# Kernel optimization log

Hardware: AMD Instinct MI355X
Metric: run time of the kernel (lower is better)

The kernel has to match this reference:

```python
import jax, jax.numpy as jnp
import numpy as np

COMMITMENT_COST = 0.25


def _l2norm(v, axis=-1, eps=1e-12):
    # matches F.normalize(p=2): v / max(||v||, eps)
    n = jnp.sqrt(jnp.sum(v * v, axis=axis, keepdims=True))
    return v / jnp.maximum(n, eps)


def setup_inputs() -> dict:
    key = jax.random.key(0)
    k1, k2 = jax.random.split(key)
    x = jax.random.normal(k1, (32768, 512), dtype=jnp.float32)
    emb_weight = jax.random.normal(k2, (8192, 512), dtype=jnp.float32)
    return {"x": x, "emb_weight": emb_weight}


def reference(x, emb_weight):
    xn = _l2norm(x)                     # [N, D]
    wn = _l2norm(emb_weight)            # [K, D]
    # squared L2 distances: ||xn||^2 + ||wn||^2 - 2 xn.wn
    dists = (jnp.sum(xn * xn, axis=-1, keepdims=True)
             + jnp.sum(wn * wn, axis=-1)
             - 2.0 * jnp.matmul(xn, wn.T))          # [N, K]
    encoding_indices = jnp.argmin(dists, axis=1)    # [N]
    quantized = _l2norm(emb_weight[encoding_indices])  # [N, D]
    q_latent_loss = jnp.mean((quantized - jax.lax.stop_gradient(xn)) ** 2)
    e_latent_loss = jnp.mean((xn - jax.lax.stop_gradient(quantized)) ** 2)
    loss = q_latent_loss + COMMITMENT_COST * e_latent_loss
    # straight-through estimator
    quantized_out = xn + jax.lax.stop_gradient(quantized - xn)
    return quantized_out, loss, encoding_indices
```

## Files before the change

kernel.cpp:

```cpp
#include <hip/hip_runtime.h>
#include <math.h>
#include <stdint.h>

#define N_Q 32768
#define K_C 8192
#define D_DIM 512
#define NSTEP 16
#define KT 64

typedef __attribute__((ext_vector_type(8))) short bf16x8;
typedef __attribute__((ext_vector_type(4))) float f32x4;
typedef unsigned long long u64;

typedef const __attribute__((address_space(1))) void gv_t;
typedef __attribute__((address_space(3))) void lv_t;

static __device__ __forceinline__ void gl16(const void* g, void* l) {
    __builtin_amdgcn_global_load_lds((gv_t*)g, (lv_t*)l, 16, 0, 0);
}

static __device__ __forceinline__ unsigned short f2bf(float f) {
    unsigned u = __float_as_uint(f);
    unsigned r = u + 0x7fffu + ((u >> 16) & 1u);
    return (unsigned short)(r >> 16);
}
static __device__ __forceinline__ float bf2f(unsigned short h) {
    return __uint_as_float(((unsigned)h) << 16);
}
static __device__ __forceinline__ unsigned fmap(float f) {
    unsigned u = __float_as_uint(f);
    return (u & 0x80000000u) ? ~u : (u | 0x80000000u);
}
static __device__ __forceinline__ float funmap(unsigned m) {
    return __uint_as_float((m & 0x80000000u) ? (m & 0x7fffffffu) : ~m);
}
static __device__ __forceinline__ u64 u64min(u64 a, u64 b) { return a < b ? a : b; }

__global__ void k_normw(const float* __restrict__ w, unsigned short* __restrict__ wh,
                        float* __restrict__ wnorm, float* __restrict__ wnorm2,
                        float* __restrict__ rho_w) {
    __shared__ float red[4];
    __shared__ float s_n;
    int k = blockIdx.x;
    int t = threadIdx.x;
    int lane = t & 63, wid = t >> 6;
    float v0 = w[(size_t)k * D_DIM + t];
    float v1 = w[(size_t)k * D_DIM + t + 256];
    float ss = fmaf(v0, v0, v1 * v1);
    for (int off = 32; off; off >>= 1) ss += __shfl_down(ss, off, 64);
    if (lane == 0) red[wid] = ss;
    __syncthreads();
    if (t == 0) s_n = fmaxf(sqrtf(red[0] + red[1] + red[2] + red[3]), 1e-12f);
    __syncthreads();
    float n = s_n;
    float a0 = v0 / n, a1 = v1 / n;
    unsigned short h0 = f2bf(a0), h1 = f2bf(a1);
    wh[(size_t)k * D_DIM + t] = h0;
    wh[(size_t)k * D_DIM + t + 256] = h1;
    float r0 = a0 - bf2f(h0), r1 = a1 - bf2f(h1);
    float s2 = fmaf(a0, a0, a1 * a1);
    float sr = fmaf(r0, r0, r1 * r1);
    for (int off = 32; off; off >>= 1) s2 += __shfl_down(s2, off, 64);
    for (int off = 32; off; off >>= 1) sr += __shfl_down(sr, off, 64);
    __syncthreads();
    if (lane == 0) red[wid] = s2;
    __syncthreads();
    float tot2 = red[0] + red[1] + red[2] + red[3];
    __syncthreads();
    if (lane == 0) red[wid] = sr;
    __syncthreads();
    if (t == 0) {
        wnorm[k] = n;
        wnorm2[k] = tot2;
        rho_w[k] = sqrtf(red[0] + red[1] + red[2] + red[3]);
    }
}

__global__ void k_wmax(const float* __restrict__ rho_w, float* __restrict__ rwmax) {
    __shared__ float red[4];
    int t = threadIdx.x, lane = t & 63, wid = t >> 6;
    float m = 0.f;
    for (int i = t; i < K_C; i += 256) m = fmaxf(m, rho_w[i]);
    for (int off = 32; off; off >>= 1) m = fmaxf(m, __shfl_down(m, off, 64));
    if (lane == 0) red[wid] = m;
    __syncthreads();
    if (t == 0) rwmax[0] = fmaxf(fmaxf(red[0], red[1]), fmaxf(red[2], red[3]));
}

__global__ void k_normx(const float* __restrict__ x, const float* __restrict__ rwmax,
                        float* __restrict__ xnorm, unsigned short* __restrict__ xh,
                        float* __restrict__ weps) {
    int wid = threadIdx.x >> 6, lane = threadIdx.x & 63;
    int n = blockIdx.x * 4 + wid;
    const float* xr = x + (size_t)n * D_DIM;
    float v[8];
    float ss = 0.f;
    #pragma unroll
    for (int i = 0; i < 8; ++i) {
        v[i] = xr[lane + i * 64];
        ss = fmaf(v[i], v[i], ss);
    }
    for (int off = 32; off; off >>= 1) ss += __shfl_down(ss, off, 64);
    ss = __shfl(ss, 0, 64);
    float nrm = fmaxf(sqrtf(ss), 1e-12f);
    float sr = 0.f;
    #pragma unroll
    for (int i = 0; i < 8; ++i) {
        float a = v[i] / nrm;
        unsigned short h = f2bf(a);
        xh[(size_t)n * D_DIM + lane + i * 64] = h;
        float r = a - bf2f(h);
        sr = fmaf(r, r, sr);
    }
    for (int off = 32; off; off >>= 1) sr += __shfl_down(sr, off, 64);
    if (lane == 0) {
        xnorm[n] = nrm;
        float rho = sqrtf(sr);
        float rwm = rwmax[0];
        weps[n] = 2.f * (2.f * (rho + (1.f + rho) * rwm) + 1.5e-4f);
    }
}

__global__ __launch_bounds__(512, 4) void k_score(
    const unsigned short* __restrict__ xh, const unsigned short* __restrict__ wh,
    const float* __restrict__ wnorm2, const float* __restrict__ weps,
    u64* __restrict__ pmin_part, unsigned char* __restrict__ cnt_part)
{
    __shared__ __align__(16) char lds[49152];
    int tid = threadIdx.x;
    int lane = tid & 63, wid = tid >> 6;
    int wm = wid >> 2, wn = wid & 3;
    int ktp = blockIdx.x;
    int k0 = ktp * 256;
    int n0 = blockIdx.y * 128;
    int c15 = lane & 15, g = lane >> 4;

    int aoff[4], boff[4];
    #pragma unroll
    for (int f = 0; f < 4; ++f) {
        int ar = wm * 64 + f * 16 + c15;
        aoff[f] = (ar * 4 + (g ^ ((ar >> 1) & 3))) * 16;
        int br = wn * 64 + f * 16 + c15;
        boff[f] = (br * 4 + (g ^ ((br >> 1) & 3))) * 16;
    }

    int ra = tid >> 2, ga = (tid & 3) ^ ((tid >> 3) & 3);
    size_t aA  = (size_t)(n0 + ra) * D_DIM + ga * 8;
    size_t aB0 = (size_t)(k0 + ra) * D_DIM + ga * 8;
    size_t aB1 = (size_t)(k0 + 128 + ra) * D_DIM + ga * 8;

    f32x4 acc[4][4];
    #pragma unroll
    for (int i = 0; i < 4; ++i)
        #pragma unroll
        for (int j = 0; j < 4; ++j) acc[i][j] = (f32x4){0.f, 0.f, 0.f, 0.f};

    gl16(xh + aA, lds + tid * 16);
    gl16(wh + aB0, lds + 8192 + tid * 16);
    gl16(wh + aB1, lds + 16384 + tid * 16);
    __syncthreads();

    for (int t = 0; t < NSTEP; ++t) {
        if (t < NSTEP - 1) {
            int du = (t + 1) * 32;
            char* nb = lds + (((t + 1) & 1) ? 24576 : 0);
            gl16(xh + aA + du, nb + tid * 16);
            gl16(wh + aB0 + du, nb + 8192 + tid * 16);
            gl16(wh + aB1 + du, nb + 16384 + tid * 16);
        }
        const char* cb = lds + ((t & 1) ? 24576 : 0);
        bf16x8 ah[4], bh[4];
        #pragma unroll
        for (int f = 0; f < 4; ++f) {
            ah[f] = *(const bf16x8*)(cb + aoff[f]);
            bh[f] = *(const bf16x8*)(cb + 8192 + boff[f]);
        }
        #pragma unroll
        for (int i = 0; i < 4; ++i)
            #pragma unroll
            for (int j = 0; j < 4; ++j)
                acc[i][j] = __builtin_amdgcn_mfma_f32_16x16x32_bf16(ah[i], bh[j], acc[i][j], 0, 0, 0);
        __syncthreads();
    }

    float w2[4];
    #pragma unroll
    for (int j = 0; j < 4; ++j) w2[j] = wnorm2[k0 + wn * 64 + j * 16 + c15];

    u64* scr = (u64*)lds;
    float* tminS = (float*)(lds + 4096);
    float* wepsS = tminS + 256;
    int* cntS = (int*)(wepsS + 128);

    #pragma unroll
    for (int m = 0; m < 4; ++m) {
        #pragma unroll
        for (int reg = 0; reg < 4; ++reg) {
            float bv = INFINITY;
            int bk = 0x7fffffff;
            #pragma unroll
            for (int j = 0; j < 4; ++j) {
                float v = fmaf(-2.f, acc[m][j][reg], w2[j]);
                int kk = k0 + wn * 64 + j * 16 + c15;
                if (v < bv || (v == bv && kk < bk)) { bv = v; bk = kk; }
            }
            for (int off = 8; off; off >>= 1) {
                float v2 = __shfl_xor(bv, off, 16);
                int k2 = __shfl_xor(bk, off, 16);
                if (v2 < bv || (v2 == bv && k2 < bk)) { bv = v2; bk = k2; }
            }
            if (c15 == 0) {
                int row = wm * 64 + m * 16 + g * 4 + reg;
                scr[row * 4 + wn] = ((u64)fmap(bv) << 32) | (unsigned)bk;
            }
        }
    }
    __syncthreads();
    if (tid < 256) {
        int row = tid >> 1, half = tid & 1;
        u64 a = scr[row * 4 + half * 2], b = scr[row * 4 + half * 2 + 1];
        u64 mn = (b < a) ? b : a;
        pmin_part[(size_t)(ktp * 2 + half) * N_Q + n0 + row] = mn;
        tminS[row * 2 + half] = funmap((unsigned)(mn >> 32));
        cntS[row * 2 + half] = 0;
    }
    if (tid >= 256 && tid < 384) wepsS[tid - 256] = weps[n0 + tid - 256];
    __syncthreads();
    {
        int half = wn >> 1;
        #pragma unroll
        for (int m = 0; m < 4; ++m) {
            #pragma unroll
            for (int reg = 0; reg < 4; ++reg) {
                int row = wm * 64 + m * 16 + g * 4 + reg;
                float thr = tminS[row * 2 + half] + wepsS[row];
                int c = 0;
                #pragma unroll
                for (int j = 0; j < 4; ++j) {
                    float v = fmaf(-2.f, acc[m][j][reg], w2[j]);
                    c += (v <= thr) ? 1 : 0;
                }
                for (int off = 8; off; off >>= 1) c += __shfl_xor(c, off, 16);
                if (c15 == 0) atomicAdd(&cntS[row * 2 + half], c);
            }
        }
    }
    __syncthreads();
    if (tid < 256) {
        int row = tid >> 1, half = tid & 1;
        int c = cntS[tid];
        cnt_part[(size_t)(ktp * 2 + half) * N_Q + n0 + row] =
            (unsigned char)(c > 255 ? 255 : c);
    }
}

__global__ void k_final(const float* __restrict__ x, const float* __restrict__ emb,
                        const float* __restrict__ xnorm, const float* __restrict__ wnorm,
                        const float* __restrict__ wnorm2, const float* __restrict__ weps,
                        const u64* __restrict__ pmin_part,
                        const unsigned char* __restrict__ cnt_part,
                        float* __restrict__ qout, float* __restrict__ idxf,
                        float* __restrict__ partials) {
    __shared__ float red[4];
    __shared__ float xs[4][D_DIM];
    int t = threadIdx.x, lane = t & 63, wid = t >> 6;
    int n = blockIdx.x * 4 + wid;

    u64 pm = pmin_part[(size_t)lane * N_Q + n];
    int cnt = cnt_part[(size_t)lane * N_Q + n];
    u64 mn = pm;
    for (int off = 32; off; off >>= 1) mn = u64min(mn, __shfl_xor(mn, off, 64));
    float thr = funmap((unsigned)(mn >> 32)) + weps[n];

    float xn = xnorm[n];
    const float4* xp = (const float4*)(x + (size_t)n * D_DIM + lane * 8);
    float4 xa = xp[0], xb = xp[1];
    xa.x /= xn; xa.y /= xn; xa.z /= xn; xa.w /= xn;
    xb.x /= xn; xb.y /= xn; xb.z /= xn; xb.w /= xn;
    *(float4*)&xs[wid][lane * 8] = xa;
    *(float4*)&xs[wid][lane * 8 + 4] = xb;

    u64 best = 0xFFFFFFFFFFFFFFFFull;
    u64 cand = __ballot(funmap((unsigned)(pm >> 32)) <= thr);
    while (cand) {
        int tt = __builtin_ctzll(cand);
        cand &= cand - 1;
        u64 pmt = __shfl(pm, tt);
        int ct = __shfl(cnt, tt);
        if (ct == 1) {
            int k = (int)(unsigned)(pmt & 0xffffffffull);
            const float4* ep = (const float4*)(emb + (size_t)k * D_DIM + lane * 8);
            float4 e0 = ep[0], e1 = ep[1];
            float dt = xa.x * e0.x + xa.y * e0.y + xa.z * e0.z + xa.w * e0.w
                     + xb.x * e1.x + xb.y * e1.y + xb.z * e1.z + xb.w * e1.w;
            for (int off = 32; off; off >>= 1) dt += __shfl_xor(dt, off, 64);
            float dist = fmaf(-2.f, dt / wnorm[k], wnorm2[k]);
            u64 pk = ((u64)fmap(dist) << 32) | (unsigned)k;
            best = u64min(best, pk);
        } else {
            #pragma unroll
            for (int pass = 0; pass < 2; ++pass) {
                int k = tt * 128 + pass * 64 + lane;
                const float4* ep = (const float4*)(emb + (size_t)k * D_DIM);
                float dt = 0.f;
                #pragma unroll 8
                for (int i = 0; i < D_DIM / 4; ++i) {
                    float4 e = ep[i];
                    dt = fmaf(xs[wid][i * 4 + 0], e.x, dt);
                    dt = fmaf(xs[wid][i * 4 + 1], e.y, dt);
                    dt = fmaf(xs[wid][i * 4 + 2], e.z, dt);
                    dt = fmaf(xs[wid][i * 4 + 3], e.w, dt);
                }
                float dist = fmaf(-2.f, dt / wnorm[k], wnorm2[k]);
                u64 pk = ((u64)fmap(dist) << 32) | (unsigned)k;
                best = u64min(best, pk);
            }
        }
    }
    for (int off = 32; off; off >>= 1) best = u64min(best, __shfl_xor(best, off, 64));

    int kk = (int)(unsigned)(best & 0xffffffffull);
    float nn = wnorm[kk];
    const float* er = emb + (size_t)kk * D_DIM + lane * 8;
    float4 e0 = *(const float4*)er;
    float4 e1 = *(const float4*)(er + 4);
    float4 q0, q1;
    q0.x = e0.x / nn; q0.y = e0.y / nn; q0.z = e0.z / nn; q0.w = e0.w / nn;
    q1.x = e1.x / nn; q1.y = e1.y / nn; q1.z = e1.z / nn; q1.w = e1.w / nn;

    float d0 = xa.x - q0.x, d1 = xa.y - q0.y, d2 = xa.z - q0.z, d3 = xa.w - q0.w;
    float d4 = xb.x - q1.x, d5 = xb.y - q1.y, d6 = xb.z - q1.z, d7 = xb.w - q1.w;
    float ds = d0 * d0 + d1 * d1 + d2 * d2 + d3 * d3
             + d4 * d4 + d5 * d5 + d6 * d6 + d7 * d7;

    float* qo = qout + (size_t)n * D_DIM + lane * 8;
    *(float4*)qo = q0;
    *(float4*)(qo + 4) = q1;
    if (lane == 0) idxf[n] = (float)kk;

    for (int off = 32; off; off >>= 1) ds += __shfl_down(ds, off, 64);
    if (lane == 0) red[wid] = ds;
    __syncthreads();
    if (t == 0) partials[blockIdx.x] = red[0] + red[1] + red[2] + red[3];
}

__global__ void k_loss(const float* __restrict__ partials, float* __restrict__ out_loss) {
    __shared__ float red[4];
    int t = threadIdx.x, lane = t & 63, wid = t >> 6;
    float s = 0.f;
    for (int i = t; i < 8192; i += 256) s += partials[i];
    for (int off = 32; off; off >>= 1) s += __shfl_down(s, off, 64);
    if (lane == 0) red[wid] = s;
    __syncthreads();
    if (t == 0)
        out_loss[0] = (red[0] + red[1] + red[2] + red[3]) * (1.25f / ((float)N_Q * (float)D_DIM));
}

extern "C" void kernel_launch(void* const* d_in, const int* in_sizes, int n_in,
                              void* d_out, int out_size, void* d_ws, size_t ws_size,
                              hipStream_t stream) {
    (void)in_sizes; (void)n_in; (void)out_size; (void)ws_size;
    const float* x = (const float*)d_in[0];
    const float* w = (const float*)d_in[1];

    float* out = (float*)d_out;
    float* qout = out;
    float* loss = out + (size_t)N_Q * D_DIM;
    float* idxf = loss + 1;

    unsigned short* xh = (unsigned short*)qout;

    char* ws = (char*)d_ws;
    unsigned short* wh = (unsigned short*)ws;
    float* wnorm2 = (float*)(wh + (size_t)K_C * D_DIM);
    float* wnorm = wnorm2 + K_C;
    float* rho_w = wnorm + K_C;
    float* rwmax = rho_w + K_C;
    float* xnorm = rwmax + 64;
    float* weps = xnorm + N_Q;
    u64* pmin_part = (u64*)(weps + N_Q);
    unsigned char* cnt_part = (unsigned char*)(pmin_part + (size_t)KT * N_Q);
    float* partials = (float*)(cnt_part + (size_t)KT * N_Q);

    k_normw<<<K_C, 256, 0, stream>>>(w, wh, wnorm, wnorm2, rho_w);
    k_wmax<<<1, 256, 0, stream>>>(rho_w, rwmax);
    k_normx<<<N_Q / 4, 256, 0, stream>>>(x, rwmax, xnorm, xh, weps);
    dim3 grid(KT / 2, N_Q / 128);
    k_score<<<grid, 512, 0, stream>>>(xh, wh, wnorm2, weps, pmin_part, cnt_part);
    k_final<<<N_Q / 4, 256, 0, stream>>>(x, w, xnorm, wnorm, wnorm2, weps,
                                         pmin_part, cnt_part, qout, idxf, partials);
    k_loss<<<1, 256, 0, stream>>>(partials, loss);
}
```

Measured before the change: 624.7 us.

## Drop LDS staging in score GEMM; load MFMA operands directly from global

The score kernel stops staging X and codebook tiles through double-buffered LDS with global_load_lds and per-step barriers. Each wave now reads its bf16 fragments straight from global memory into registers. Tiles shrink to 64 query rows by 256 codes per 256-thread block, and the epilogue is adapted to match. This removes the LDS round trip and the syncthreads in the K loop. In exchange, operands are no longer shared across waves, so each wave re-reads the X tile from global or cache, and the 16-byte strided row loads are less coalesced.

```diff
diff --git a/kernel.cpp b/kernel.cpp
--- a/kernel.cpp
+++ b/kernel.cpp
@@ -11,13 +11,6 @@
 typedef __attribute__((ext_vector_type(8))) short bf16x8;
 typedef __attribute__((ext_vector_type(4))) float f32x4;
 typedef unsigned long long u64;
-
-typedef const __attribute__((address_space(1))) void gv_t;
-typedef __attribute__((address_space(3))) void lv_t;
-
-static __device__ __forceinline__ void gl16(const void* g, void* l) {
-    __builtin_amdgcn_global_load_lds((gv_t*)g, (lv_t*)l, 16, 0, 0);
-}
 
 static __device__ __forceinline__ unsigned short f2bf(float f) {
     unsigned u = __float_as_uint(f);
@@ -121,33 +114,31 @@
     }
 }
 
-__global__ __launch_bounds__(512, 4) void k_score(
+__global__ __launch_bounds__(256, 4) void k_score(
     const unsigned short* __restrict__ xh, const unsigned short* __restrict__ wh,
     const float* __restrict__ wnorm2, const float* __restrict__ weps,
     u64* __restrict__ pmin_part, unsigned char* __restrict__ cnt_part)
 {
-    __shared__ __align__(16) char lds[49152];
+    __shared__ u64 scr[64 * 4];
+    __shared__ float tminS[64 * 2];
+    __shared__ float wepsS[64];
+    __shared__ int cntS[64 * 2];
+
     int tid = threadIdx.x;
-    int lane = tid & 63, wid = tid >> 6;
-    int wm = wid >> 2, wn = wid & 3;
+    int lane = tid & 63, w = tid >> 6;
     int ktp = blockIdx.x;
+    int n0 = blockIdx.y * 64;
     int k0 = ktp * 256;
-    int n0 = blockIdx.y * 128;
+    int kw = k0 + w * 64;
     int c15 = lane & 15, g = lane >> 4;
 
-    int aoff[4], boff[4];
+    const unsigned short* ap[4];
+    const unsigned short* bp[4];
     #pragma unroll
     for (int f = 0; f < 4; ++f) {
-        int ar = wm * 64 + f * 16 + c15;
-        aoff[f] = (ar * 4 + (g ^ ((ar >> 1) & 3))) * 16;
-        int br = wn * 64 + f * 16 + c15;
-        boff[f] = (br * 4 + (g ^ ((br >> 1) & 3))) * 16;
-    }
-
-    int ra = tid >> 2, ga = (tid & 3) ^ ((tid >> 3) & 3);
-    size_t aA  = (size_t)(n0 + ra) * D_DIM + ga * 8;
-    size_t aB0 = (size_t)(k0 + ra) * D_DIM + ga * 8;
-    size_t aB1 = (size_t)(k0 + 128 + ra) * D_DIM + ga * 8;
+        ap[f] = xh + (size_t)(n0 + f * 16 + c15) * D_DIM + g * 8;
+        bp[f] = wh + (size_t)(kw + f * 16 + c15) * D_DIM + g * 8;
+    }
 
     f32x4 acc[4][4];
     #pragma unroll
@@ -155,42 +146,24 @@
         #pragma unroll
         for (int j = 0; j < 4; ++j) acc[i][j] = (f32x4){0.f, 0.f, 0.f, 0.f};
 
-    gl16(xh + aA, lds + tid * 16);
-    gl16(wh + aB0, lds + 8192 + tid * 16);
-    gl16(wh + aB1, lds + 16384 + tid * 16);
-    __syncthreads();
-
+    #pragma unroll
     for (int t = 0; t < NSTEP; ++t) {
-        if (t < NSTEP - 1) {
-            int du = (t + 1) * 32;
-            char* nb = lds + (((t + 1) & 1) ? 24576 : 0);
-            gl16(xh + aA + du, nb + tid * 16);
-            gl16(wh + aB0 + du, nb + 8192 + tid * 16);
-            gl16(wh + aB1 + du, nb + 16384 + tid * 16);
-        }
-        const char* cb = lds + ((t & 1) ? 24576 : 0);
         bf16x8 ah[4], bh[4];
         #pragma unroll
         for (int f = 0; f < 4; ++f) {
-            ah[f] = *(const bf16x8*)(cb + aoff[f]);
-            bh[f] = *(const bf16x8*)(cb + 8192 + boff[f]);
+            ah[f] = *(const bf16x8*)(ap[f] + t * 32);
+            bh[f] = *(const bf16x8*)(bp[f] + t * 32);
         }
         #pragma unroll
         for (int i = 0; i < 4; ++i)
             #pragma unroll
             for (int j = 0; j < 4; ++j)
                 acc[i][j] = __builtin_amdgcn_mfma_f32_16x16x32_bf16(ah[i], bh[j], acc[i][j], 0, 0, 0);
-        __syncthreads();
     }
 
     float w2[4];
     #pragma unroll
-    for (int j = 0; j < 4; ++j) w2[j] = wnorm2[k0 + wn * 64 + j * 16 + c15];
-
-    u64* scr = (u64*)lds;
-    float* tminS = (float*)(lds + 4096);
-    float* wepsS = tminS + 256;
-    int* cntS = (int*)(wepsS + 128);
+    for (int j = 0; j < 4; ++j) w2[j] = wnorm2[kw + j * 16 + c15];
 
     #pragma unroll
     for (int m = 0; m < 4; ++m) {
@@ -201,7 +174,7 @@
             #pragma unroll
             for (int j = 0; j < 4; ++j) {
                 float v = fmaf(-2.f, acc[m][j][reg], w2[j]);
-                int kk = k0 + wn * 64 + j * 16 + c15;
+                int kk = kw + j * 16 + c15;
                 if (v < bv || (v == bv && kk < bk)) { bv = v; bk = kk; }
             }
             for (int off = 8; off; off >>= 1) {
@@ -210,13 +183,14 @@
                 if (v2 < bv || (v2 == bv && k2 < bk)) { bv = v2; bk = k2; }
             }
             if (c15 == 0) {
-                int row = wm * 64 + m * 16 + g * 4 + reg;
-                scr[row * 4 + wn] = ((u64)fmap(bv) << 32) | (unsigned)bk;
+                int row = m * 16 + g * 4 + reg;
+                scr[row * 4 + w] = ((u64)fmap(bv) << 32) | (unsigned)bk;
             }
         }
     }
-    __syncthreads();
-    if (tid < 256) {
+    if (tid < 64) wepsS[tid] = weps[n0 + tid];
+    __syncthreads();
+    if (tid < 128) {
         int row = tid >> 1, half = tid & 1;
         u64 a = scr[row * 4 + half * 2], b = scr[row * 4 + half * 2 + 1];
         u64 mn = (b < a) ? b : a;
@@ -224,15 +198,14 @@
         tminS[row * 2 + half] = funmap((unsigned)(mn >> 32));
         cntS[row * 2 + half] = 0;
     }
-    if (tid >= 256 && tid < 384) wepsS[tid - 256] = weps[n0 + tid - 256];
     __syncthreads();
     {
-        int half = wn >> 1;
+        int half = w >> 1;
         #pragma unroll
         for (int m = 0; m < 4; ++m) {
             #pragma unroll
             for (int reg = 0; reg < 4; ++reg) {
-                int row = wm * 64 + m * 16 + g * 4 + reg;
+                int row = m * 16 + g * 4 + reg;
                 float thr = tminS[row * 2 + half] + wepsS[row];
                 int c = 0;
                 #pragma unroll
@@ -246,9 +219,9 @@
         }
     }
     __syncthreads();
-    if (tid < 256) {
+    if (tid < 128) {
         int row = tid >> 1, half = tid & 1;
-        int c = cntS[tid];
+        int c = cntS[row * 2 + half];
         cnt_part[(size_t)(ktp * 2 + half) * N_Q + n0 + row] =
             (unsigned char)(c > 255 ? 255 : c);
     }
@@ -385,8 +358,8 @@
     k_normw<<<K_C, 256, 0, stream>>>(w, wh, wnorm, wnorm2, rho_w);
     k_wmax<<<1, 256, 0, stream>>>(rho_w, rwmax);
     k_normx<<<N_Q / 4, 256, 0, stream>>>(x, rwmax, xnorm, xh, weps);
-    dim3 grid(KT / 2, N_Q / 128);
-    k_score<<<grid, 512, 0, stream>>>(xh, wh, wnorm2, weps, pmin_part, cnt_part);
+    dim3 grid(32, N_Q / 64);
+    k_score<<<grid, 256, 0, stream>>>(xh, wh, wnorm2, weps, pmin_part, cnt_part);
     k_final<<<N_Q / 4, 256, 0, stream>>>(x, w, xnorm, wnorm, wnorm2, weps,
                                          pmin_part, cnt_part, qout, idxf, partials);
     k_loss<<<1, 256, 0, stream>>>(partials, loss);
```

New measurement: 1.122 ms. 1.8x slower.

## Track top-2 candidates per tile so refinement handles two-candidate tiles cheaply

Applied to the files above, without the earlier changes.

The score kernel now keeps the best two packed (distance, index) keys per row and tile, merging them across lanes and waves, and writes the second-best index to a new workspace array. The final kernel uses it so that tiles with up to two near-threshold candidates are rescored with one or two wave-wide dot products instead of a brute-force fp32 rescan of all 128 codes in the tile. The bf16 codebook copy moves into the output buffer to make room for the new array. This costs extra shuffles and LDS traffic in the score epilogue plus an extra 4 bytes per row and tile of global writes and reads.

```diff
diff --git a/kernel.cpp b/kernel.cpp
--- a/kernel.cpp
+++ b/kernel.cpp
@@ -35,6 +35,7 @@
     return __uint_as_float((m & 0x80000000u) ? (m & 0x7fffffffu) : ~m);
 }
 static __device__ __forceinline__ u64 u64min(u64 a, u64 b) { return a < b ? a : b; }
+static __device__ __forceinline__ u64 u64max(u64 a, u64 b) { return a > b ? a : b; }
 
 __global__ void k_normw(const float* __restrict__ w, unsigned short* __restrict__ wh,
                         float* __restrict__ wnorm, float* __restrict__ wnorm2,
@@ -124,7 +125,8 @@
 __global__ __launch_bounds__(512, 4) void k_score(
     const unsigned short* __restrict__ xh, const unsigned short* __restrict__ wh,
     const float* __restrict__ wnorm2, const float* __restrict__ weps,
-    u64* __restrict__ pmin_part, unsigned char* __restrict__ cnt_part)
+    u64* __restrict__ pmin_part, unsigned* __restrict__ idx2_part,
+    unsigned char* __restrict__ cnt_part)
 {
     __shared__ __align__(16) char lds[49152];
     int tid = threadIdx.x;
@@ -187,8 +189,9 @@
     #pragma unroll
     for (int j = 0; j < 4; ++j) w2[j] = wnorm2[k0 + wn * 64 + j * 16 + c15];
 
-    u64* scr = (u64*)lds;
-    float* tminS = (float*)(lds + 4096);
+    u64* scr  = (u64*)lds;
+    u64* scr2 = scr + 512;
+    float* tminS = (float*)(scr2 + 512);
     float* wepsS = tminS + 256;
     int* cntS = (int*)(wepsS + 128);
 
@@ -196,32 +199,40 @@
     for (int m = 0; m < 4; ++m) {
         #pragma unroll
         for (int reg = 0; reg < 4; ++reg) {
-            float bv = INFINITY;
-            int bk = 0x7fffffff;
+            u64 t1 = 0xFFFFFFFFFFFFFFFFull, t2 = 0xFFFFFFFFFFFFFFFFull;
             #pragma unroll
             for (int j = 0; j < 4; ++j) {
                 float v = fmaf(-2.f, acc[m][j][reg], w2[j]);
                 int kk = k0 + wn * 64 + j * 16 + c15;
-                if (v < bv || (v == bv && kk < bk)) { bv = v; bk = kk; }
-            }
+                u64 pk = ((u64)fmap(v) << 32) | (unsigned)kk;
+                if (pk < t1) { t2 = t1; t1 = pk; }
+                else if (pk < t2) { t2 = pk; }
+            }
+            #pragma unroll
             for (int off = 8; off; off >>= 1) {
-                float v2 = __shfl_xor(bv, off, 16);
-                int k2 = __shfl_xor(bk, off, 16);
-                if (v2 < bv || (v2 == bv && k2 < bk)) { bv = v2; bk = k2; }
+                u64 q1 = __shfl_xor(t1, off, 16);
+                u64 q2 = __shfl_xor(t2, off, 16);
+                u64 m1 = u64min(t1, q1);
+                u64 m2 = u64min(u64max(t1, q1), u64min(t2, q2));
+                t1 = m1; t2 = m2;
             }
             if (c15 == 0) {
                 int row = wm * 64 + m * 16 + g * 4 + reg;
-                scr[row * 4 + wn] = ((u64)fmap(bv) << 32) | (unsigned)bk;
+                scr[row * 4 + wn] = t1;
+                scr2[row * 4 + wn] = t2;
             }
         }
     }
     __syncthreads();
     if (tid < 256) {
         int row = tid >> 1, half = tid & 1;
-        u64 a = scr[row * 4 + half * 2], b = scr[row * 4 + half * 2 + 1];
-        u64 mn = (b < a) ? b : a;
-        pmin_part[(size_t)(ktp * 2 + half) * N_Q + n0 + row] = mn;
-        tminS[row * 2 + half] = funmap((unsigned)(mn >> 32));
+        u64 a1 = scr[row * 4 + half * 2], b1 = scr[row * 4 + half * 2 + 1];
+        u64 a2 = scr2[row * 4 + half * 2], b2 = scr2[row * 4 + half * 2 + 1];
+        u64 m1 = u64min(a1, b1);
+        u64 m2 = u64min(u64max(a1, b1), u64min(a2, b2));
+        pmin_part[(size_t)(ktp * 2 + half) * N_Q + n0 + row] = m1;
+        idx2_part[(size_t)(ktp * 2 + half) * N_Q + n0 + row] = (unsigned)(m2 & 0xffffffffull);
+        tminS[row * 2 + half] = funmap((unsigned)(m1 >> 32));
         cntS[row * 2 + half] = 0;
     }
     if (tid >= 256 && tid < 384) wepsS[tid - 256] = weps[n0 + tid - 256];
@@ -258,6 +269,7 @@
                         const float* __restrict__ xnorm, const float* __restrict__ wnorm,
                         const float* __restrict__ wnorm2, const float* __restrict__ weps,
                         const u64* __restrict__ pmin_part,
+                        const unsigned* __restrict__ idx2_part,
                         const unsigned char* __restrict__ cnt_part,
                         float* __restrict__ qout, float* __restrict__ idxf,
                         float* __restrict__ partials) {
@@ -268,6 +280,7 @@
 
     u64 pm = pmin_part[(size_t)lane * N_Q + n];
     int cnt = cnt_part[(size_t)lane * N_Q + n];
+    unsigned i2 = idx2_part[(size_t)lane * N_Q + n];
     u64 mn = pm;
     for (int off = 32; off; off >>= 1) mn = u64min(mn, __shfl_xor(mn, off, 64));
     float thr = funmap((unsigned)(mn >> 32)) + weps[n];
@@ -287,16 +300,19 @@
         cand &= cand - 1;
         u64 pmt = __shfl(pm, tt);
         int ct = __shfl(cnt, tt);
-        if (ct == 1) {
+        if (ct <= 2) {
             int k = (int)(unsigned)(pmt & 0xffffffffull);
-            const float4* ep = (const float4*)(emb + (size_t)k * D_DIM + lane * 8);
-            float4 e0 = ep[0], e1 = ep[1];
-            float dt = xa.x * e0.x + xa.y * e0.y + xa.z * e0.z + xa.w * e0.w
-                     + xb.x * e1.x + xb.y * e1.y + xb.z * e1.z + xb.w * e1.w;
-            for (int off = 32; off; off >>= 1) dt += __shfl_xor(dt, off, 64);
-            float dist = fmaf(-2.f, dt / wnorm[k], wnorm2[k]);
-            u64 pk = ((u64)fmap(dist) << 32) | (unsigned)k;
-            best = u64min(best, pk);
+            for (int e = 0; e < ct; ++e) {
+                const float4* ep = (const float4*)(emb + (size_t)k * D_DIM + lane * 8);
+                float4 e0 = ep[0], e1 = ep[1];
+                float dt = xa.x * e0.x + xa.y * e0.y + xa.z * e0.z + xa.w * e0.w
+                         + xb.x * e1.x + xb.y * e1.y + xb.z * e1.z + xb.w * e1.w;
+                for (int off = 32; off; off >>= 1) dt += __shfl_xor(dt, off, 64);
+                float dist = fmaf(-2.f, dt / wnorm[k], wnorm2[k]);
+                u64 pk = ((u64)fmap(dist) << 32) | (unsigned)k;
+                best = u64min(best, pk);
+                k = (int)__shfl(i2, tt);
+            }
         } else {
             #pragma unroll
             for (int pass = 0; pass < 2; ++pass) {
@@ -369,25 +385,27 @@
     float* idxf = loss + 1;
 
     unsigned short* xh = (unsigned short*)qout;
+    unsigned short* wh = xh + (size_t)N_Q * D_DIM;
 
     char* ws = (char*)d_ws;
-    unsigned short* wh = (unsigned short*)ws;
-    float* wnorm2 = (float*)(wh + (size_t)K_C * D_DIM);
+    float* wnorm2 = (float*)ws;
     float* wnorm = wnorm2 + K_C;
     float* rho_w = wnorm + K_C;
     float* rwmax = rho_w + K_C;
     float* xnorm = rwmax + 64;
     float* weps = xnorm + N_Q;
     u64* pmin_part = (u64*)(weps + N_Q);
-    unsigned char* cnt_part = (unsigned char*)(pmin_part + (size_t)KT * N_Q);
+    unsigned* idx2_part = (unsigned*)(pmin_part + (size_t)KT * N_Q);
+    unsigned char* cnt_part = (unsigned char*)(idx2_part + (size_t)KT * N_Q);
     float* partials = (float*)(cnt_part + (size_t)KT * N_Q);
 
     k_normw<<<K_C, 256, 0, stream>>>(w, wh, wnorm, wnorm2, rho_w);
     k_wmax<<<1, 256, 0, stream>>>(rho_w, rwmax);
     k_normx<<<N_Q / 4, 256, 0, stream>>>(x, rwmax, xnorm, xh, weps);
     dim3 grid(KT / 2, N_Q / 128);
-    k_score<<<grid, 512, 0, stream>>>(xh, wh, wnorm2, weps, pmin_part, cnt_part);
+    k_score<<<grid, 512, 0, stream>>>(xh, wh, wnorm2, weps, pmin_part, idx2_part, cnt_part);
     k_final<<<N_Q / 4, 256, 0, stream>>>(x, w, xnorm, wnorm, wnorm2, weps,
-                                         pmin_part, cnt_part, qout, idxf, partials);
+                                         pmin_part, idx2_part, cnt_part,
+                                         qout, idxf, partials);
     k_loss<<<1, 256, 0, stream>>>(partials, loss);
 }
```

New measurement: 641.9 us. 1.03x slower.
